# Performance work log

Measured on AMD Instinct MI355X. Metric: run time of the kernel, lower is better.

The kernel has to match this reference:

```python
import jax, jax.numpy as jnp
import numpy as np

BRANCH = [True, False] * 10  # branchLs: joints that also emit a tracking frame
TRACK_IDX = np.where(np.array(BRANCH))[0]


def rpy2r(rpy):
    # rpy (..., 3) -> rotation (..., 3, 3), R = Rz(yaw) @ Ry(pitch) @ Rx(roll)
    r, p, y = rpy[..., 0], rpy[..., 1], rpy[..., 2]
    cr, sr = jnp.cos(r), jnp.sin(r)
    cp, sp = jnp.cos(p), jnp.sin(p)
    cy, sy = jnp.cos(y), jnp.sin(y)
    return jnp.stack([
        jnp.stack([cy * cp, cy * sp * sr - sy * cr, cy * sp * cr + sy * sr], -1),
        jnp.stack([sy * cp, sy * sp * sr + cy * cr, sy * sp * cr - cy * sr], -1),
        jnp.stack([-sp, cp * sr, cp * cr], -1)], -2)


def pr2t(p, R):
    # p (...,3), R (...,3,3) -> homogeneous transform (...,4,4)
    top = jnp.concatenate([R, p[..., None]], axis=-1)
    bot = jnp.broadcast_to(jnp.array([0., 0., 0., 1.], R.dtype), top.shape[:-2] + (1, 4))
    return jnp.concatenate([top, bot], axis=-2)


def rodrigues(axis, q):
    # axis (J,3) (normalized inside), q (B,J) angles -> (B,J,3,3)
    a = axis / (jnp.linalg.norm(axis, axis=-1, keepdims=True) + 1e-12)
    ax, ay, az = a[..., 0], a[..., 1], a[..., 2]
    z = jnp.zeros_like(ax)
    K = jnp.stack([jnp.stack([z, -az, ay], -1),
                   jnp.stack([az, z, -ax], -1),
                   jnp.stack([-ay, ax, z], -1)], -2)  # (J,3,3)
    K2 = K @ K
    s = jnp.sin(q)[..., None, None]  # (B,J,1,1)
    c = jnp.cos(q)[..., None, None]
    return jnp.eye(3, dtype=q.dtype) + s * K + (1. - c) * K2


def _forward(rev_q, pri_q, rev_p_off, rev_rpy_off, pri_p_off, pri_rpy_off,
             rev_axis, pri_axis, p_track, rpy_track):
    B, J = rev_q.shape
    dt = rev_q.dtype
    rev_T_off = pr2t(rev_p_off, rpy2r(rev_rpy_off))    # (J,4,4)
    pri_T_off = pr2t(pri_p_off, rpy2r(pri_rpy_off))    # (J,4,4)
    T_track = pr2t(p_track, rpy2r(rpy_track))          # (J,4,4)
    rev_T = pr2t(jnp.zeros((B, J, 3), dt), rodrigues(rev_axis, rev_q))  # (B,J,4,4)
    eye3 = jnp.broadcast_to(jnp.eye(3, dtype=dt), (B, J, 3, 3))
    pri_T = pr2t(pri_q[..., None] * pri_axis[None], eye3)               # (B,J,4,4)
    # fold constant offsets into per-joint steps, joint axis leading for scan
    rev_step = jnp.einsum('jab,njbc->jnac', rev_T_off, rev_T)  # (J,B,4,4)
    pri_step = jnp.einsum('jab,njbc->jnac', pri_T_off, pri_T)  # (J,B,4,4)

    def step(out, xs):
        rs, ps, tt = xs
        out1 = out @ rs          # after revolute joint
        out2 = out1 @ ps         # after prismatic joint
        return out2, (out1, out2, out2 @ tt)

    init = jnp.broadcast_to(jnp.eye(4, dtype=dt), (B, 4, 4))
    _, (rev_all, pri_all, trk_all) = jax.lax.scan(step, init, (rev_step, pri_step, T_track))
    RevSE3 = jnp.transpose(rev_all, (1, 0, 2, 3))                  # (B,J,4,4)
    PriSE3 = jnp.transpose(pri_all, (1, 0, 2, 3))                  # (B,J,4,4)
    TrackingSE3 = jnp.transpose(trk_all[TRACK_IDX], (1, 0, 2, 3))  # (B,n_track,4,4)
    return TrackingSE3, RevSE3, PriSE3


def setup_inputs() -> dict:
    key = jax.random.key(0)
    ks = jax.random.split(key, 10)
    B, J = 32768, 20
    u = lambda k, s: jax.random.uniform(k, s, jnp.float32, -1., 1.)
    return {
        'rev_q_value': jax.random.normal(ks[0], (B, J), jnp.float32),
        'pri_q_value': jax.random.normal(ks[1], (B, J), jnp.float32),
        'rev_p_offset': u(ks[2], (J, 3)), 'rev_rpy_offset': u(ks[3], (J, 3)),
        'pri_p_offset': u(ks[4], (J, 3)), 'pri_rpy_offset': u(ks[5], (J, 3)),
        'rev_axis': u(ks[6], (J, 3)), 'pri_axis': u(ks[7], (J, 3)),
        'p_track': u(ks[8], (J, 3)), 'rpy_track': u(ks[9], (J, 3)),
    }


def reference(rev_q_value, pri_q_value, rev_p_offset, rev_rpy_offset,
              pri_p_offset, pri_rpy_offset, rev_axis, pri_axis, p_track, rpy_track):
    return _forward(rev_q_value, pri_q_value, rev_p_offset, rev_rpy_offset,
                    pri_p_offset, pri_rpy_offset, rev_axis, pri_axis, p_track, rpy_track)
```

## Files before the change

### kernel.cpp

```cpp
#include <hip/hip_runtime.h>
#include <math.h>


constexpr int NJ = 20;
constexpr int BPB = 8;

struct Aff { float R[9]; float p[3]; };

__device__ __forceinline__ void rpy2r_dev(float r, float p, float y, float R[9]) {
    float sr, cr, sp, cp, sy, cy;
    __sincosf(r, &sr, &cr);
    __sincosf(p, &sp, &cp);
    __sincosf(y, &sy, &cy);
    R[0] = cy * cp; R[1] = cy * sp * sr - sy * cr; R[2] = cy * sp * cr + sy * sr;
    R[3] = sy * cp; R[4] = sy * sp * sr + cy * cr; R[5] = sy * sp * cr - cy * sr;
    R[6] = -sp;     R[7] = cp * sr;                R[8] = cp * cr;
}

__device__ __forceinline__ void mat33_mul(const float A[9], const float B[9], float C[9]) {
#pragma unroll
    for (int i = 0; i < 3; ++i) {
        C[3 * i + 0] = A[3 * i + 0] * B[0] + A[3 * i + 1] * B[3] + A[3 * i + 2] * B[6];
        C[3 * i + 1] = A[3 * i + 0] * B[1] + A[3 * i + 1] * B[4] + A[3 * i + 2] * B[7];
        C[3 * i + 2] = A[3 * i + 0] * B[2] + A[3 * i + 1] * B[5] + A[3 * i + 2] * B[8];
    }
}

__device__ __forceinline__ Aff compose(const Aff& A, const Aff& B) {
    Aff C;
    mat33_mul(A.R, B.R, C.R);
#pragma unroll
    for (int i = 0; i < 3; ++i)
        C.p[i] = fmaf(A.R[3 * i + 0], B.p[0],
                 fmaf(A.R[3 * i + 1], B.p[1],
                 fmaf(A.R[3 * i + 2], B.p[2], A.p[i])));
    return C;
}

__device__ __forceinline__ Aff shfl_up_aff(const Aff& V, int d) {
    Aff N;
#pragma unroll
    for (int k = 0; k < 9; ++k) N.R[k] = __shfl_up(V.R[k], d, 32);
#pragma unroll
    for (int k = 0; k < 3; ++k) N.p[k] = __shfl_up(V.p[k], d, 32);
    return N;
}

__global__ __launch_bounds__(256) void fk_scan_kernel(
    const float* __restrict__ rev_q,      const float* __restrict__ pri_q,
    const float* __restrict__ rev_p_off,  const float* __restrict__ rev_rpy_off,
    const float* __restrict__ pri_p_off,  const float* __restrict__ pri_rpy_off,
    const float* __restrict__ rev_axis,   const float* __restrict__ pri_axis,
    const float* __restrict__ p_track,    const float* __restrict__ rpy_track,
    float* __restrict__ out, int B)
{
    __shared__ float4 cst[NJ][11];
    const int t = threadIdx.x;

    if (t < NJ) {
        const int j = t;
        float Ro[9], Rp[9], Rt[9];
        rpy2r_dev(rev_rpy_off[3 * j], rev_rpy_off[3 * j + 1], rev_rpy_off[3 * j + 2], Ro);
        rpy2r_dev(pri_rpy_off[3 * j], pri_rpy_off[3 * j + 1], pri_rpy_off[3 * j + 2], Rp);
        rpy2r_dev(rpy_track[3 * j],   rpy_track[3 * j + 1],   rpy_track[3 * j + 2],   Rt);
        cst[j][0] = make_float4(Ro[0], Ro[1], Ro[2], rev_p_off[3 * j + 0]);
        cst[j][1] = make_float4(Ro[3], Ro[4], Ro[5], rev_p_off[3 * j + 1]);
        cst[j][2] = make_float4(Ro[6], Ro[7], Ro[8], rev_p_off[3 * j + 2]);
        cst[j][3] = make_float4(Rp[0], Rp[1], Rp[2], pri_p_off[3 * j + 0]);
        cst[j][4] = make_float4(Rp[3], Rp[4], Rp[5], pri_p_off[3 * j + 1]);
        cst[j][5] = make_float4(Rp[6], Rp[7], Rp[8], pri_p_off[3 * j + 2]);
        cst[j][6] = make_float4(Rt[0], Rt[1], Rt[2], p_track[3 * j + 0]);
        cst[j][7] = make_float4(Rt[3], Rt[4], Rt[5], p_track[3 * j + 1]);
        cst[j][8] = make_float4(Rt[6], Rt[7], Rt[8], p_track[3 * j + 2]);
        const float ax = rev_axis[3 * j], ay = rev_axis[3 * j + 1], az = rev_axis[3 * j + 2];
        const float inv = 1.0f / (sqrtf(ax * ax + ay * ay + az * az) + 1e-12f);
        cst[j][9] = make_float4(ax * inv, ay * inv, az * inv, 0.0f);
        const float px = pri_axis[3 * j], py = pri_axis[3 * j + 1], pz = pri_axis[3 * j + 2];
        cst[j][10] = make_float4(Rp[0] * px + Rp[1] * py + Rp[2] * pz,
                                 Rp[3] * px + Rp[4] * py + Rp[5] * pz,
                                 Rp[6] * px + Rp[7] * py + Rp[8] * pz, 0.0f);
    }
    __syncthreads();

    const int j = t & 31;
    const int b = blockIdx.x * BPB + (t >> 5);
    if (j >= NJ || b >= B) return;

    const float rq = rev_q[(size_t)b * NJ + j];
    const float pq = pri_q[(size_t)b * NJ + j];

    float s, c;
    __sincosf(rq, &s, &c);
    const float4 a4 = cst[j][9];
    const float ax = a4.x, ay = a4.y, az = a4.z, omc = 1.0f - c;
    float Rr[9];
    Rr[0] = c + omc * ax * ax;      Rr[1] = omc * ax * ay - s * az; Rr[2] = omc * ax * az + s * ay;
    Rr[3] = omc * ax * ay + s * az; Rr[4] = c + omc * ay * ay;      Rr[5] = omc * ay * az - s * ax;
    Rr[6] = omc * ax * az - s * ay; Rr[7] = omc * ay * az + s * ax; Rr[8] = c + omc * az * az;

    const float4 cr0 = cst[j][0], cr1 = cst[j][1], cr2 = cst[j][2];
    const float Roff[9] = {cr0.x, cr0.y, cr0.z, cr1.x, cr1.y, cr1.z, cr2.x, cr2.y, cr2.z};
    Aff revstep;
    mat33_mul(Roff, Rr, revstep.R);
    revstep.p[0] = cr0.w; revstep.p[1] = cr1.w; revstep.p[2] = cr2.w;

    const float4 cp0 = cst[j][3], cp1 = cst[j][4], cp2 = cst[j][5];
    const float4 w4 = cst[j][10];
    const float Rpoff[9] = {cp0.x, cp0.y, cp0.z, cp1.x, cp1.y, cp1.z, cp2.x, cp2.y, cp2.z};
    const float pp[3] = {fmaf(pq, w4.x, cp0.w), fmaf(pq, w4.y, cp1.w), fmaf(pq, w4.z, cp2.w)};

    Aff V;
    mat33_mul(revstep.R, Rpoff, V.R);
#pragma unroll
    for (int i = 0; i < 3; ++i)
        V.p[i] = fmaf(revstep.R[3 * i + 0], pp[0],
                 fmaf(revstep.R[3 * i + 1], pp[1],
                 fmaf(revstep.R[3 * i + 2], pp[2], revstep.p[i])));

#pragma unroll
    for (int d = 1; d < 32; d <<= 1) {
        Aff N = shfl_up_aff(V, d);
        if (j >= d) V = compose(N, V);
    }

    Aff P = shfl_up_aff(V, 1);
    if (j == 0) {
        P.R[0] = 1.f; P.R[1] = 0.f; P.R[2] = 0.f;
        P.R[3] = 0.f; P.R[4] = 1.f; P.R[5] = 0.f;
        P.R[6] = 0.f; P.R[7] = 0.f; P.R[8] = 1.f;
        P.p[0] = 0.f; P.p[1] = 0.f; P.p[2] = 0.f;
    }
    const Aff Rev = compose(P, revstep);

    float4* out4 = reinterpret_cast<float4*>(out);
    const float4 bot = make_float4(0.f, 0.f, 0.f, 1.f);

    const size_t revBase = (size_t)B * 40 + (size_t)b * 80 + (size_t)j * 4;
    out4[revBase + 0] = make_float4(Rev.R[0], Rev.R[1], Rev.R[2], Rev.p[0]);
    out4[revBase + 1] = make_float4(Rev.R[3], Rev.R[4], Rev.R[5], Rev.p[1]);
    out4[revBase + 2] = make_float4(Rev.R[6], Rev.R[7], Rev.R[8], Rev.p[2]);
    out4[revBase + 3] = bot;

    const size_t priBase = (size_t)B * 120 + (size_t)b * 80 + (size_t)j * 4;
    out4[priBase + 0] = make_float4(V.R[0], V.R[1], V.R[2], V.p[0]);
    out4[priBase + 1] = make_float4(V.R[3], V.R[4], V.R[5], V.p[1]);
    out4[priBase + 2] = make_float4(V.R[6], V.R[7], V.R[8], V.p[2]);
    out4[priBase + 3] = bot;

    if ((j & 1) == 0) {
        const float4 ct0 = cst[j][6], ct1 = cst[j][7], ct2 = cst[j][8];
        Aff T;
        T.R[0] = ct0.x; T.R[1] = ct0.y; T.R[2] = ct0.z;
        T.R[3] = ct1.x; T.R[4] = ct1.y; T.R[5] = ct1.z;
        T.R[6] = ct2.x; T.R[7] = ct2.y; T.R[8] = ct2.z;
        T.p[0] = ct0.w; T.p[1] = ct1.w; T.p[2] = ct2.w;
        const Aff Trk = compose(V, T);
        const size_t tb = (size_t)b * 40 + (size_t)(j >> 1) * 4;
        out4[tb + 0] = make_float4(Trk.R[0], Trk.R[1], Trk.R[2], Trk.p[0]);
        out4[tb + 1] = make_float4(Trk.R[3], Trk.R[4], Trk.R[5], Trk.p[1]);
        out4[tb + 2] = make_float4(Trk.R[6], Trk.R[7], Trk.R[8], Trk.p[2]);
        out4[tb + 3] = bot;
    }
}

extern "C" void kernel_launch(void* const* d_in, const int* in_sizes, int n_in,
                              void* d_out, int out_size, void* d_ws, size_t ws_size,
                              hipStream_t stream) {
    (void)n_in; (void)out_size; (void)d_ws; (void)ws_size;
    const float* rev_q       = (const float*)d_in[0];
    const float* pri_q       = (const float*)d_in[1];
    const float* rev_p_off   = (const float*)d_in[2];
    const float* rev_rpy_off = (const float*)d_in[3];
    const float* pri_p_off   = (const float*)d_in[4];
    const float* pri_rpy_off = (const float*)d_in[5];
    const float* rev_axis    = (const float*)d_in[6];
    const float* pri_axis    = (const float*)d_in[7];
    const float* p_track     = (const float*)d_in[8];
    const float* rpy_track   = (const float*)d_in[9];

    const int B = in_sizes[0] / NJ;
    const int blocks = (B + BPB - 1) / BPB;
    fk_scan_kernel<<<dim3(blocks), dim3(256), 0, stream>>>(
        rev_q, pri_q, rev_p_off, rev_rpy_off, pri_p_off, pri_rpy_off,
        rev_axis, pri_axis, p_track, rpy_track, (float*)d_out, B);
}
```

Before: 149.9 us.

## Stage FK outputs in shared memory for coalesced nontemporal stores

Results for each block's 8 batch rows are written into a padded LDS staging buffer. All 256 threads then write the contiguous output regions with coalesced float4 nontemporal stores, instead of each lane scattering strided 64-byte rows. This targets write efficiency on a store-bound kernel. It adds an extra barrier and LDS traffic. It also drops the tail bounds check by assuming B is divisible by 8.

```diff
diff --git a/kernel.cpp b/kernel.cpp
--- a/kernel.cpp
+++ b/kernel.cpp
@@ -2,8 +2,13 @@
 #include <math.h>
 
 
-constexpr int NJ = 20;
-constexpr int BPB = 8;
+constexpr int NJ  = 20;
+constexpr int GB  = 8;
+constexpr int BSTR = 151;
+constexpr int PRIO = 60;
+constexpr int TRKO = 120;
+
+typedef float v4f __attribute__((ext_vector_type(4)));
 
 struct Aff { float R[9]; float p[3]; };
 
@@ -46,7 +51,7 @@
     return N;
 }
 
-__global__ __launch_bounds__(256) void fk_scan_kernel(
+__global__ __launch_bounds__(256) void fk_kernel(
     const float* __restrict__ rev_q,      const float* __restrict__ pri_q,
     const float* __restrict__ rev_p_off,  const float* __restrict__ rev_rpy_off,
     const float* __restrict__ pri_p_off,  const float* __restrict__ pri_rpy_off,
@@ -55,6 +60,7 @@
     float* __restrict__ out, int B)
 {
     __shared__ float4 cst[NJ][11];
+    __shared__ v4f stg[GB * BSTR];
     const int t = threadIdx.x;
 
     if (t < NJ) {
@@ -83,83 +89,113 @@
     __syncthreads();
 
     const int j = t & 31;
-    const int b = blockIdx.x * BPB + (t >> 5);
-    if (j >= NJ || b >= B) return;
-
-    const float rq = rev_q[(size_t)b * NJ + j];
-    const float pq = pri_q[(size_t)b * NJ + j];
-
-    float s, c;
-    __sincosf(rq, &s, &c);
-    const float4 a4 = cst[j][9];
-    const float ax = a4.x, ay = a4.y, az = a4.z, omc = 1.0f - c;
-    float Rr[9];
-    Rr[0] = c + omc * ax * ax;      Rr[1] = omc * ax * ay - s * az; Rr[2] = omc * ax * az + s * ay;
-    Rr[3] = omc * ax * ay + s * az; Rr[4] = c + omc * ay * ay;      Rr[5] = omc * ay * az - s * ax;
-    Rr[6] = omc * ax * az - s * ay; Rr[7] = omc * ay * az + s * ax; Rr[8] = c + omc * az * az;
-
-    const float4 cr0 = cst[j][0], cr1 = cst[j][1], cr2 = cst[j][2];
-    const float Roff[9] = {cr0.x, cr0.y, cr0.z, cr1.x, cr1.y, cr1.z, cr2.x, cr2.y, cr2.z};
-    Aff revstep;
-    mat33_mul(Roff, Rr, revstep.R);
-    revstep.p[0] = cr0.w; revstep.p[1] = cr1.w; revstep.p[2] = cr2.w;
-
-    const float4 cp0 = cst[j][3], cp1 = cst[j][4], cp2 = cst[j][5];
-    const float4 w4 = cst[j][10];
-    const float Rpoff[9] = {cp0.x, cp0.y, cp0.z, cp1.x, cp1.y, cp1.z, cp2.x, cp2.y, cp2.z};
-    const float pp[3] = {fmaf(pq, w4.x, cp0.w), fmaf(pq, w4.y, cp1.w), fmaf(pq, w4.z, cp2.w)};
-
-    Aff V;
-    mat33_mul(revstep.R, Rpoff, V.R);
-#pragma unroll
-    for (int i = 0; i < 3; ++i)
-        V.p[i] = fmaf(revstep.R[3 * i + 0], pp[0],
-                 fmaf(revstep.R[3 * i + 1], pp[1],
-                 fmaf(revstep.R[3 * i + 2], pp[2], revstep.p[i])));
-
-#pragma unroll
-    for (int d = 1; d < 32; d <<= 1) {
-        Aff N = shfl_up_aff(V, d);
-        if (j >= d) V = compose(N, V);
-    }
-
-    Aff P = shfl_up_aff(V, 1);
-    if (j == 0) {
-        P.R[0] = 1.f; P.R[1] = 0.f; P.R[2] = 0.f;
-        P.R[3] = 0.f; P.R[4] = 1.f; P.R[5] = 0.f;
-        P.R[6] = 0.f; P.R[7] = 0.f; P.R[8] = 1.f;
-        P.p[0] = 0.f; P.p[1] = 0.f; P.p[2] = 0.f;
-    }
-    const Aff Rev = compose(P, revstep);
-
-    float4* out4 = reinterpret_cast<float4*>(out);
-    const float4 bot = make_float4(0.f, 0.f, 0.f, 1.f);
-
-    const size_t revBase = (size_t)B * 40 + (size_t)b * 80 + (size_t)j * 4;
-    out4[revBase + 0] = make_float4(Rev.R[0], Rev.R[1], Rev.R[2], Rev.p[0]);
-    out4[revBase + 1] = make_float4(Rev.R[3], Rev.R[4], Rev.R[5], Rev.p[1]);
-    out4[revBase + 2] = make_float4(Rev.R[6], Rev.R[7], Rev.R[8], Rev.p[2]);
-    out4[revBase + 3] = bot;
-
-    const size_t priBase = (size_t)B * 120 + (size_t)b * 80 + (size_t)j * 4;
-    out4[priBase + 0] = make_float4(V.R[0], V.R[1], V.R[2], V.p[0]);
-    out4[priBase + 1] = make_float4(V.R[3], V.R[4], V.R[5], V.p[1]);
-    out4[priBase + 2] = make_float4(V.R[6], V.R[7], V.R[8], V.p[2]);
-    out4[priBase + 3] = bot;
-
-    if ((j & 1) == 0) {
-        const float4 ct0 = cst[j][6], ct1 = cst[j][7], ct2 = cst[j][8];
-        Aff T;
-        T.R[0] = ct0.x; T.R[1] = ct0.y; T.R[2] = ct0.z;
-        T.R[3] = ct1.x; T.R[4] = ct1.y; T.R[5] = ct1.z;
-        T.R[6] = ct2.x; T.R[7] = ct2.y; T.R[8] = ct2.z;
-        T.p[0] = ct0.w; T.p[1] = ct1.w; T.p[2] = ct2.w;
-        const Aff Trk = compose(V, T);
-        const size_t tb = (size_t)b * 40 + (size_t)(j >> 1) * 4;
-        out4[tb + 0] = make_float4(Trk.R[0], Trk.R[1], Trk.R[2], Trk.p[0]);
-        out4[tb + 1] = make_float4(Trk.R[3], Trk.R[4], Trk.R[5], Trk.p[1]);
-        out4[tb + 2] = make_float4(Trk.R[6], Trk.R[7], Trk.R[8], Trk.p[2]);
-        out4[tb + 3] = bot;
+    const int g = t >> 5;
+    const int b = blockIdx.x * GB + g;
+
+    if (j < NJ) {
+        const float rq = rev_q[(size_t)b * NJ + j];
+        const float pq = pri_q[(size_t)b * NJ + j];
+
+        float s, c;
+        __sincosf(rq, &s, &c);
+        const float4 a4 = cst[j][9];
+        const float ax = a4.x, ay = a4.y, az = a4.z, omc = 1.0f - c;
+        float Rr[9];
+        Rr[0] = c + omc * ax * ax;      Rr[1] = omc * ax * ay - s * az; Rr[2] = omc * ax * az + s * ay;
+        Rr[3] = omc * ax * ay + s * az; Rr[4] = c + omc * ay * ay;      Rr[5] = omc * ay * az - s * ax;
+        Rr[6] = omc * ax * az - s * ay; Rr[7] = omc * ay * az + s * ax; Rr[8] = c + omc * az * az;
+
+        const float4 cr0 = cst[j][0], cr1 = cst[j][1], cr2 = cst[j][2];
+        const float Roff[9] = {cr0.x, cr0.y, cr0.z, cr1.x, cr1.y, cr1.z, cr2.x, cr2.y, cr2.z};
+        Aff revstep;
+        mat33_mul(Roff, Rr, revstep.R);
+        revstep.p[0] = cr0.w; revstep.p[1] = cr1.w; revstep.p[2] = cr2.w;
+
+        const float4 cp0 = cst[j][3], cp1 = cst[j][4], cp2 = cst[j][5];
+        const float4 w4 = cst[j][10];
+        const float Rpoff[9] = {cp0.x, cp0.y, cp0.z, cp1.x, cp1.y, cp1.z, cp2.x, cp2.y, cp2.z};
+        const float pp[3] = {fmaf(pq, w4.x, cp0.w), fmaf(pq, w4.y, cp1.w), fmaf(pq, w4.z, cp2.w)};
+
+        Aff V;
+        mat33_mul(revstep.R, Rpoff, V.R);
+#pragma unroll
+        for (int i = 0; i < 3; ++i)
+            V.p[i] = fmaf(revstep.R[3 * i + 0], pp[0],
+                     fmaf(revstep.R[3 * i + 1], pp[1],
+                     fmaf(revstep.R[3 * i + 2], pp[2], revstep.p[i])));
+
+#pragma unroll
+        for (int d = 1; d < 32; d <<= 1) {
+            Aff N = shfl_up_aff(V, d);
+            if (j >= d) V = compose(N, V);
+        }
+
+        Aff P = shfl_up_aff(V, 1);
+        if (j == 0) {
+            P.R[0] = 1.f; P.R[1] = 0.f; P.R[2] = 0.f;
+            P.R[3] = 0.f; P.R[4] = 1.f; P.R[5] = 0.f;
+            P.R[6] = 0.f; P.R[7] = 0.f; P.R[8] = 1.f;
+            P.p[0] = 0.f; P.p[1] = 0.f; P.p[2] = 0.f;
+        }
+        const Aff Rev = compose(P, revstep);
+
+        v4f* sg = &stg[g * BSTR];
+        sg[3 * j + 0] = (v4f){Rev.R[0], Rev.R[1], Rev.R[2], Rev.p[0]};
+        sg[3 * j + 1] = (v4f){Rev.R[3], Rev.R[4], Rev.R[5], Rev.p[1]};
+        sg[3 * j + 2] = (v4f){Rev.R[6], Rev.R[7], Rev.R[8], Rev.p[2]};
+        sg[PRIO + 3 * j + 0] = (v4f){V.R[0], V.R[1], V.R[2], V.p[0]};
+        sg[PRIO + 3 * j + 1] = (v4f){V.R[3], V.R[4], V.R[5], V.p[1]};
+        sg[PRIO + 3 * j + 2] = (v4f){V.R[6], V.R[7], V.R[8], V.p[2]};
+
+        if ((j & 1) == 0) {
+            const float4 ct0 = cst[j][6], ct1 = cst[j][7], ct2 = cst[j][8];
+            Aff T;
+            T.R[0] = ct0.x; T.R[1] = ct0.y; T.R[2] = ct0.z;
+            T.R[3] = ct1.x; T.R[4] = ct1.y; T.R[5] = ct1.z;
+            T.R[6] = ct2.x; T.R[7] = ct2.y; T.R[8] = ct2.z;
+            T.p[0] = ct0.w; T.p[1] = ct1.w; T.p[2] = ct2.w;
+            const Aff Trk = compose(V, T);
+            const int jt = j >> 1;
+            sg[TRKO + 3 * jt + 0] = (v4f){Trk.R[0], Trk.R[1], Trk.R[2], Trk.p[0]};
+            sg[TRKO + 3 * jt + 1] = (v4f){Trk.R[3], Trk.R[4], Trk.R[5], Trk.p[1]};
+            sg[TRKO + 3 * jt + 2] = (v4f){Trk.R[6], Trk.R[7], Trk.R[8], Trk.p[2]};
+        }
+    }
+    __syncthreads();
+
+    v4f* out4 = reinterpret_cast<v4f*>(out);
+    const v4f bot = (v4f){0.f, 0.f, 0.f, 1.f};
+    const int blockBase = blockIdx.x * GB;
+
+    {
+        v4f* dst = out4 + (size_t)blockBase * 40;
+#pragma unroll
+        for (int k = t; k < GB * 40; k += 256) {
+            const int gg = k / 40, w = k - gg * 40;
+            const int jt = w >> 2, r = w & 3;
+            const v4f v = (r == 3) ? bot : stg[gg * BSTR + TRKO + 3 * jt + r];
+            __builtin_nontemporal_store(v, &dst[k]);
+        }
+    }
+    {
+        v4f* dst = out4 + (size_t)B * 40 + (size_t)blockBase * 80;
+#pragma unroll
+        for (int k = t; k < GB * 80; k += 256) {
+            const int gg = k / 80, w = k - gg * 80;
+            const int jj = w >> 2, r = w & 3;
+            const v4f v = (r == 3) ? bot : stg[gg * BSTR + 3 * jj + r];
+            __builtin_nontemporal_store(v, &dst[k]);
+        }
+    }
+    {
+        v4f* dst = out4 + (size_t)B * 120 + (size_t)blockBase * 80;
+#pragma unroll
+        for (int k = t; k < GB * 80; k += 256) {
+            const int gg = k / 80, w = k - gg * 80;
+            const int jj = w >> 2, r = w & 3;
+            const v4f v = (r == 3) ? bot : stg[gg * BSTR + PRIO + 3 * jj + r];
+            __builtin_nontemporal_store(v, &dst[k]);
+        }
     }
 }
 
@@ -179,8 +215,8 @@
     const float* rpy_track   = (const float*)d_in[9];
 
     const int B = in_sizes[0] / NJ;
-    const int blocks = (B + BPB - 1) / BPB;
-    fk_scan_kernel<<<dim3(blocks), dim3(256), 0, stream>>>(
+    const int blocks = B / GB;
+    fk_kernel<<<dim3(blocks), dim3(256), 0, stream>>>(
         rev_q, pri_q, rev_p_off, rev_rpy_off, pri_p_off, pri_rpy_off,
         rev_axis, pri_axis, p_track, rpy_track, (float*)d_out, B);
 }
```

Measured after the change: 139.2 us. 1.08x faster.
